# Performance work log

Measured on AMD Instinct MI355X. Metric: run time of the kernel, lower is better.

Reference implementation:

```python
import jax, jax.numpy as jnp
import numpy as np

G, N_PER_G, V, H, DIN, DOUT, E = 1024, 64, 32, 128, 128, 10, 1048576
N = G * N_PER_G


def _lin(key, fan_in, fan_out):
    k1, k2 = jax.random.split(key)
    s = 1.0 / np.sqrt(fan_in)
    return (jax.random.uniform(k1, (fan_in, fan_out), jnp.float32, -s, s),
            jax.random.uniform(k2, (fan_out,), jnp.float32, -s, s))


def setup_inputs() -> dict:
    key = jax.random.key(0)
    ks = jax.random.split(key, 16)
    x = jax.random.normal(ks[0], (N, DIN), jnp.float32)
    # random edges constrained within each graph's contiguous node block
    gid = jax.random.randint(ks[1], (E,), 0, G)
    src = gid * N_PER_G + jax.random.randint(ks[2], (E,), 0, N_PER_G)
    dst = gid * N_PER_G + jax.random.randint(ks[3], (E,), 0, N_PER_G)
    edge_index = jnp.stack([src, dst]).astype(jnp.int64)
    batch = jnp.repeat(jnp.arange(G, dtype=jnp.int64), N_PER_G)
    edge_weights = jnp.ones((G, N_PER_G, V), jnp.float32) / V  # uniform init
    vemb = jax.random.normal(ks[4], (G, V, H), jnp.float32)
    vemb = vemb / jnp.linalg.norm(vemb, axis=-1, keepdims=True)
    W_emb, b_emb = _lin(ks[5], DIN, H)
    W_gcn, b_gcn = _lin(ks[6], H, H)
    aff_W1, aff_b1 = _lin(ks[7], H, H)
    aff_W2, aff_b2 = _lin(ks[8], H, H)
    vn_W1, vn_b1 = _lin(ks[9], H, H)
    vn_W2, vn_b2 = _lin(ks[10], H, H)
    mlp_W1, mlp_b1 = _lin(ks[11], H, H)
    mlp_W2, mlp_b2 = _lin(ks[12], H, DOUT)
    return dict(x=x, edge_index=edge_index, batch=batch, edge_weights=edge_weights,
                vemb=vemb, W_emb=W_emb, b_emb=b_emb, W_gcn=W_gcn, b_gcn=b_gcn,
                aff_W1=aff_W1, aff_b1=aff_b1, aff_W2=aff_W2, aff_b2=aff_b2,
                vn_W1=vn_W1, vn_b1=vn_b1, vn_W2=vn_W2, vn_b2=vn_b2,
                mlp_W1=mlp_W1, mlp_b1=mlp_b1, mlp_W2=mlp_W2, mlp_b2=mlp_b2)


def reference(x, edge_index, batch, edge_weights, vemb, W_emb, b_emb, W_gcn, b_gcn,
              aff_W1, aff_b1, aff_W2, aff_b2, vn_W1, vn_b1, vn_W2, vn_b2,
              mlp_W1, mlp_b1, mlp_W2, mlp_b2):
    n_nodes = x.shape[0]
    g, n, v = edge_weights.shape
    h = x @ W_emb + b_emb                                   # node embedding
    # GCNConv with self-loops and symmetric normalization
    hw = h @ W_gcn
    sl = jnp.arange(n_nodes)
    s = jnp.concatenate([edge_index[0], sl])
    d = jnp.concatenate([edge_index[1], sl])
    deg = jax.ops.segment_sum(jnp.ones_like(d, dtype=h.dtype), d, num_segments=n_nodes)
    inv = jax.lax.rsqrt(jnp.maximum(deg, 1.0))
    msg = hw[s] * (inv[s] * inv[d])[:, None]                # [E+N, H]
    h = jax.nn.relu(jax.ops.segment_sum(msg, d, num_segments=n_nodes) + b_gcn)
    # affinity MLP
    aff = jax.nn.relu(h @ aff_W1 + aff_b1) @ aff_W2 + aff_b2
    hg = h.reshape(g, n, -1)
    affg = aff.reshape(g, n, -1)
    # attention vs fixed normalized virtual-node embeddings
    att = jnp.einsum('gnh,gvh->gnv', affg, vemb) / jnp.sqrt(jnp.asarray(hg.shape[-1], h.dtype))
    ew = edge_weights * (1.0 + jax.nn.sigmoid(att))
    rs = ew.sum(axis=-1, keepdims=True)
    ew = ew / jnp.where(rs == 0, 1.0, rs)                   # row-normalize
    vn = jnp.einsum('gnv,gnh->gvh', ew, hg)                 # weighted scatter-pool
    vn = jax.nn.relu(vn @ vn_W1 + vn_b1) @ vn_W2 + vn_b2
    gf = vn.mean(axis=1)                                    # [G, H]
    return jax.nn.relu(gf @ mlp_W1 + mlp_b1) @ mlp_W2 + mlp_b2
```

## Files before the change

### kernel.cpp

```cpp
#include <hip/hip_runtime.h>
#include <hip/hip_bf16.h>
#include <cstddef>


#define EDGES 1048576
#define TS 72
#define AS 64
#define VS 136
#define BS 40

typedef __attribute__((ext_vector_type(8))) short short8;
typedef __attribute__((ext_vector_type(4))) float f32x4;
typedef __hip_bfloat16 bf;
struct __align__(8) bf4 { bf v[4]; };

__device__ __forceinline__ int foff(int nt, int ks, int l15, int kofs) {
    return (nt * 4 + ks) * 512 + l15 * 32 + kofs;
}

__global__ __launch_bounds__(256) void conv(
    const float* __restrict__ W_emb, const float* __restrict__ W_gcn,
    const float* __restrict__ b_emb, const float* __restrict__ aff_W1,
    const float* __restrict__ vn_W1, const float* __restrict__ vn_W2,
    const float* __restrict__ aff_W2,
    bf* __restrict__ gWb, bf* __restrict__ gW2f, float* __restrict__ bfold,
    unsigned* __restrict__ Cnt)
{
    int b = blockIdx.x, t = threadIdx.x;
    if (b < 4) {
        __shared__ float we[32 * 128];
        int k0 = b * 32;
        for (int i = t; i < 4096; i += 256) we[i] = W_emb[k0 * 128 + i];
        __syncthreads();
        int kk = t >> 3, jg = t & 7;
        float acc[16] = {};
        for (int m = 0; m < 128; ++m) {
            float a = we[kk * 128 + m];
            const float4* wr = (const float4*)(W_gcn + m * 128 + jg * 16);
            float4 w0 = wr[0], w1 = wr[1], w2 = wr[2], w3 = wr[3];
            acc[0]  += a * w0.x; acc[1]  += a * w0.y; acc[2]  += a * w0.z; acc[3]  += a * w0.w;
            acc[4]  += a * w1.x; acc[5]  += a * w1.y; acc[6]  += a * w1.z; acc[7]  += a * w1.w;
            acc[8]  += a * w2.x; acc[9]  += a * w2.y; acc[10] += a * w2.z; acc[11] += a * w2.w;
            acc[12] += a * w3.x; acc[13] += a * w3.y; acc[14] += a * w3.z; acc[15] += a * w3.w;
        }
        int k = k0 + kk;
        for (int jj = 0; jj < 16; ++jj) {
            int j = jg * 16 + jj;
            int off = ((j >> 4) * 4 + (k >> 5)) * 512 + (j & 15) * 32 + (k & 31);
            gWb[off] = __float2bfloat16(acc[jj]);
        }
    } else if (b == 4) {
        if (t < 128) {
            float acc = 0.f;
            for (int m = 0; m < 128; ++m) acc += b_emb[m] * W_gcn[m * 128 + t];
            bfold[t] = acc;
        }
        for (int i = t; i < 1024; i += 256) Cnt[i] = 0u;
    } else if (b < 8) {
        const float* src = (b == 5) ? aff_W1 : (b == 6) ? vn_W1 : vn_W2;
        bf* dst = gWb + (size_t)(b - 4) * 16384;
        for (int i = t; i < 16384; i += 256) {
            int n = i >> 7, k = i & 127;
            int off = ((n >> 4) * 4 + (k >> 5)) * 512 + (n & 15) * 32 + (k & 31);
            dst[off] = __float2bfloat16(src[k * 128 + n]);
        }
    } else {
        for (int i = t; i < 16384; i += 256) {
            int n = i >> 7, k = i & 127;
            int off = ((n >> 4) * 4 + (k >> 5)) * 512 + (n & 15) * 32 + (k & 31);
            gW2f[off] = __float2bfloat16(aff_W2[n * 128 + k]);
        }
    }
}

__global__ __launch_bounds__(256) void scat(const int* __restrict__ ei,
                                            unsigned* __restrict__ Cnt,
                                            unsigned short* __restrict__ sorted)
{
    __shared__ unsigned lh[1024];
    __shared__ unsigned sBase[1024];
    int t = threadIdx.x, b = blockIdx.x;
    for (int i = t; i < 1024; i += 256) lh[i] = 0;
    __syncthreads();
    unsigned er[16];
    int base = b * 4096;
#pragma unroll
    for (int i = 0; i < 16; ++i) {
        int e = base + i * 256 + t;
        int s = ei[e], d = ei[EDGES + e];
        unsigned g = (unsigned)s >> 6;
        er[i] = (g << 12) | (unsigned)((d & 63) << 6) | (unsigned)(s & 63);
        atomicAdd(&lh[g], 1u);
    }
    __syncthreads();
    for (int i = t; i < 1024; i += 256) {
        unsigned c = lh[i];
        if (c) sBase[i] = atomicAdd(&Cnt[i], c);
    }
    __syncthreads();
    for (int i = t; i < 1024; i += 256) lh[i] = 0;
    __syncthreads();
#pragma unroll
    for (int i = 0; i < 16; ++i) {
        unsigned g = er[i] >> 12;
        unsigned r = atomicAdd(&lh[g], 1u);
        unsigned p = sBase[g] + r;
        if (p < 2048) sorted[(size_t)g * 2048 + p] = (unsigned short)(er[i] & 0xFFFu);
    }
}

__global__ __launch_bounds__(256) void prepS(
    const float* __restrict__ vemb, const float* __restrict__ aff_b2,
    const bf* __restrict__ gW2f, bf* __restrict__ gS, float* __restrict__ gbatt)
{
    __shared__ __align__(16) bf sV[32 * VS];
    const int t = threadIdx.x, g = blockIdx.x;
    const int wv = t >> 6, lane = t & 63, l15 = lane & 15, q = lane >> 4;
    const int kofs = q * 8;
    const float4* gv = (const float4*)(vemb + (size_t)g * 4096);
#pragma unroll
    for (int tt = 0; tt < 4; ++tt) {
        int i = t + tt * 256;
        int v = i >> 5, o4 = i & 31;
        float4 w = gv[i];
        bf4 tv;
        tv.v[0] = __float2bfloat16(w.x); tv.v[1] = __float2bfloat16(w.y);
        tv.v[2] = __float2bfloat16(w.z); tv.v[3] = __float2bfloat16(w.w);
        *(bf4*)(sV + v * VS + o4 * 4) = tv;
    }
    __syncthreads();
    {
        int v = t >> 3, sg = t & 7;
        float s = 0.f;
        const bf* pv = sV + v * VS + sg * 16;
        const float* pb = aff_b2 + sg * 16;
#pragma unroll
        for (int o = 0; o < 16; ++o) s += pb[o] * __bfloat162float(pv[o]);
        s += __shfl_xor(s, 1); s += __shfl_xor(s, 2); s += __shfl_xor(s, 4);
        if (sg == 0) gbatt[g * 32 + v] = s;
    }
    {
        const int mt = wv & 1, nb = (wv >> 1) * 4;
        f32x4 acc[4] = {};
#pragma unroll
        for (int ks = 0; ks < 4; ++ks) {
            short8 a = *(const short8*)(sV + (mt * 16 + l15) * VS + ks * 32 + kofs);
#pragma unroll
            for (int nt = 0; nt < 4; ++nt) {
                short8 bb = *(const short8*)(gW2f + foff(nb + nt, ks, l15, kofs));
                acc[nt] = __builtin_amdgcn_mfma_f32_16x16x32_bf16(a, bb, acc[nt], 0, 0, 0);
            }
        }
#pragma unroll
        for (int nt = 0; nt < 4; ++nt)
#pragma unroll
            for (int r = 0; r < 4; ++r) {
                int v = mt * 16 + q * 4 + r;
                int k = (nb + nt) * 16 + l15;
                int off = ((v >> 4) * 4 + (k >> 5)) * 512 + (v & 15) * 32 + (k & 31);
                gS[(size_t)g * 4096 + off] = __float2bfloat16(acc[nt][r]);
            }
    }
}

__device__ __forceinline__ void gemmA8(const short8 A[4], const bf* __restrict__ gW,
                                       int l15, int kofs, f32x4 acc[8])
{
#pragma unroll
    for (int hf = 0; hf < 2; ++hf) {
        short8 b[4], bn[4];
#pragma unroll
        for (int nt = 0; nt < 4; ++nt)
            b[nt] = *(const short8*)(gW + foff(hf * 4 + nt, 0, l15, kofs));
#pragma unroll
        for (int ks = 0; ks < 4; ++ks) {
            if (ks < 3)
#pragma unroll
                for (int nt = 0; nt < 4; ++nt)
                    bn[nt] = *(const short8*)(gW + foff(hf * 4 + nt, ks + 1, l15, kofs));
#pragma unroll
            for (int nt = 0; nt < 4; ++nt)
                acc[hf * 4 + nt] = __builtin_amdgcn_mfma_f32_16x16x32_bf16(
                    A[ks], b[nt], acc[hf * 4 + nt], 0, 0, 0);
#pragma unroll
            for (int nt = 0; nt < 4; ++nt) b[nt] = bn[nt];
        }
    }
}

__device__ __forceinline__ void gemmA4(const short8 A[4], const bf* __restrict__ gW,
                                       int ntb, int l15, int kofs, f32x4 acc[4])
{
    short8 b[4], bn[4];
#pragma unroll
    for (int nt = 0; nt < 4; ++nt)
        b[nt] = *(const short8*)(gW + foff(ntb + nt, 0, l15, kofs));
#pragma unroll
    for (int ks = 0; ks < 4; ++ks) {
        if (ks < 3)
#pragma unroll
            for (int nt = 0; nt < 4; ++nt)
                bn[nt] = *(const short8*)(gW + foff(ntb + nt, ks + 1, l15, kofs));
#pragma unroll
        for (int nt = 0; nt < 4; ++nt)
            acc[nt] = __builtin_amdgcn_mfma_f32_16x16x32_bf16(A[ks], b[nt], acc[nt], 0, 0, 0);
#pragma unroll
        for (int nt = 0; nt < 4; ++nt) b[nt] = bn[nt];
    }
}

__device__ __forceinline__ void bounceA(const float vals[8][4], bf* slab,
                                        int q, int l15, short8 A[4])
{
#pragma unroll
    for (int ks = 0; ks < 4; ++ks) {
#pragma unroll
        for (int h = 0; h < 2; ++h)
#pragma unroll
            for (int r = 0; r < 4; ++r)
                slab[(q * 4 + r) * BS + h * 16 + l15] = __float2bfloat16(vals[ks * 2 + h][r]);
        A[ks] = *(const short8*)(slab + l15 * BS + q * 8);
    }
}

__global__ __launch_bounds__(256, 4) void fused_graph(
    const float* __restrict__ x, const float* __restrict__ edge_w,
    const bf* __restrict__ gWb, const float* __restrict__ bfold,
    const float* __restrict__ b_gcn, const float* __restrict__ aff_b1,
    const float* __restrict__ vn_b1, const float* __restrict__ vn_b2,
    const bf* __restrict__ gS, const float* __restrict__ gbatt,
    const unsigned short* __restrict__ sorted, const unsigned* __restrict__ Cnt,
    float* __restrict__ gfout)
{
    __shared__ __align__(16) bf sT [128 * TS];
    __shared__ __align__(16) bf sAdj[64 * AS];
    __shared__ __align__(16) bf sBounce[4 * 16 * BS];
    __shared__ __align__(16) bf sVn[32 * VS];
    __shared__ float sInv[64];

    const int tid = threadIdx.x;
    const int g = blockIdx.x;
    const int wv = tid >> 6;
    const int lane = tid & 63;
    const int l15 = lane & 15;
    const int q = lane >> 4;
    const int kofs = q * 8;
    bf* slab = sBounce + wv * (16 * BS);
    float* sGfp = (float*)sBounce;
    unsigned* cnt = (unsigned*)sVn;

    {
        uint4* c4 = (uint4*)cnt;
        c4[tid] = make_uint4(0, 0, 0, 0);
    }
    __syncthreads();
    {
        unsigned ecnt = Cnt[g]; if (ecnt > 2048) ecnt = 2048;
        const unsigned short* seg = sorted + (size_t)g * 2048;
        for (unsigned i = tid; i < ecnt; i += 256) {
            unsigned w = seg[i];
            atomicAdd(&cnt[(w >> 6) * 16 + ((w & 63u) >> 2)], 1u << ((w & 3u) * 8));
        }
    }
    __syncthreads();
    {
        int row = tid >> 2, q4 = tid & 3;
        float rs = 0.f;
#pragma unroll
        for (int w4 = 0; w4 < 4; ++w4) {
            unsigned wd = cnt[row * 16 + q4 * 4 + w4];
            bf4 tv;
#pragma unroll
            for (int j = 0; j < 4; ++j) {
                int c = (q4 * 4 + w4) * 4 + j;
                float v = (float)((wd >> (j * 8)) & 255u) + (c == row ? 1.f : 0.f);
                rs += v;
                tv.v[j] = __float2bfloat16(v);
            }
            *(bf4*)(sAdj + row * AS + (q4 * 4 + w4) * 4) = tv;
        }
        rs += __shfl_xor(rs, 1);
        rs += __shfl_xor(rs, 2);
        if (q4 == 0) sInv[row] = rsqrtf(rs);
    }
    __syncthreads();

    {
        const float4* xrow = (const float4*)(x + ((size_t)g * 64 + 16 * wv + l15) * 128);
        short8 A[4];
#pragma unroll
        for (int ks = 0; ks < 4; ++ks) {
            float4 a0 = xrow[ks * 8 + q * 2];
            float4 a1 = xrow[ks * 8 + q * 2 + 1];
            union { short8 v; bf e[8]; } u;
            u.e[0] = __float2bfloat16(a0.x); u.e[1] = __float2bfloat16(a0.y);
            u.e[2] = __float2bfloat16(a0.z); u.e[3] = __float2bfloat16(a0.w);
            u.e[4] = __float2bfloat16(a1.x); u.e[5] = __float2bfloat16(a1.y);
            u.e[6] = __float2bfloat16(a1.z); u.e[7] = __float2bfloat16(a1.w);
            A[ks] = u.v;
        }
        f32x4 acc[8] = {};
        gemmA8(A, gWb, l15, kofs, acc);
        float bf_[8];
#pragma unroll
        for (int nt = 0; nt < 8; ++nt) bf_[nt] = bfold[nt * 16 + l15];
        float iv[4];
#pragma unroll
        for (int r = 0; r < 4; ++r) iv[r] = sInv[16 * wv + q * 4 + r];
#pragma unroll
        for (int nt = 0; nt < 8; ++nt) {
            bf4 tv;
#pragma unroll
            for (int r = 0; r < 4; ++r)
                tv.v[r] = __float2bfloat16((acc[nt][r] + bf_[nt]) * iv[r]);
            *(bf4*)(sT + (nt * 16 + l15) * TS + 16 * wv + q * 4) = tv;
        }
    }
    __syncthreads();

    float hvals[8][4];
    {
        f32x4 acc[8] = {};
#pragma unroll
        for (int ks = 0; ks < 2; ++ks) {
            short8 a = *(const short8*)(sAdj + (16 * wv + l15) * AS + ks * 32 + kofs);
#pragma unroll
            for (int nt = 0; nt < 8; ++nt) {
                short8 bb = *(const short8*)(sT + (nt * 16 + l15) * TS + ks * 32 + kofs);
                acc[nt] = __builtin_amdgcn_mfma_f32_16x16x32_bf16(a, bb, acc[nt], 0, 0, 0);
            }
        }
        float iv[4];
#pragma unroll
        for (int r = 0; r < 4; ++r) iv[r] = sInv[16 * wv + q * 4 + r];
#pragma unroll
        for (int nt = 0; nt < 8; ++nt) {
            float bg = b_gcn[nt * 16 + l15];
#pragma unroll
            for (int r = 0; r < 4; ++r)
                hvals[nt][r] = fmaxf(acc[nt][r] * iv[r] + bg, 0.f);
        }
    }
    __syncthreads();

    short8 Ah[4];
    {
#pragma unroll
        for (int nt = 0; nt < 8; ++nt) {
            bf4 tv;
#pragma unroll
            for (int r = 0; r < 4; ++r) tv.v[r] = __float2bfloat16(hvals[nt][r]);
            *(bf4*)(sT + (nt * 16 + l15) * TS + 16 * wv + q * 4) = tv;
        }
        bounceA(hvals, slab, q, l15, Ah);
    }

    short8 Aa[4];
    {
        f32x4 acc[8] = {};
        gemmA8(Ah, gWb + 16384, l15, kofs, acc);
        float av[8][4];
#pragma unroll
        for (int nt = 0; nt < 8; ++nt) {
            float ba = aff_b1[nt * 16 + l15];
#pragma unroll
            for (int r = 0; r < 4; ++r) av[nt][r] = fmaxf(acc[nt][r] + ba, 0.f);
        }
        bounceA(av, slab, q, l15, Aa);
    }

    {
        short8 Sf[8];
#pragma unroll
        for (int nt = 0; nt < 2; ++nt)
#pragma unroll
            for (int ks = 0; ks < 4; ++ks)
                Sf[nt * 4 + ks] = *(const short8*)(gS + (size_t)g * 4096 + foff(nt, ks, l15, kofs));
        float ewv[2][4];
#pragma unroll
        for (int nt = 0; nt < 2; ++nt)
#pragma unroll
            for (int r = 0; r < 4; ++r)
                ewv[nt][r] = edge_w[(size_t)g * 2048 + (16 * wv + q * 4 + r) * 32 + nt * 16 + l15];
        float bt[2] = { gbatt[g * 32 + l15], gbatt[g * 32 + 16 + l15] };
        f32x4 acc[2] = {};
#pragma unroll
        for (int ks = 0; ks < 4; ++ks) {
            acc[0] = __builtin_amdgcn_mfma_f32_16x16x32_bf16(Aa[ks], Sf[ks],     acc[0], 0, 0, 0);
            acc[1] = __builtin_amdgcn_mfma_f32_16x16x32_bf16(Aa[ks], Sf[4 + ks], acc[1], 0, 0, 0);
        }
        const float sc = 0.08838834764831845f;
        float e[2][4];
#pragma unroll
        for (int r = 0; r < 4; ++r) {
#pragma unroll
            for (int nt = 0; nt < 2; ++nt) {
                float att = (acc[nt][r] + bt[nt]) * sc;
                e[nt][r] = ewv[nt][r] * (1.f + 1.f / (1.f + __expf(-att)));
            }
            float rs = e[0][r] + e[1][r];
            rs += __shfl_xor(rs, 1); rs += __shfl_xor(rs, 2);
            rs += __shfl_xor(rs, 4); rs += __shfl_xor(rs, 8);
            float ri = (rs == 0.f) ? 1.f : 1.f / rs;
            e[0][r] *= ri; e[1][r] *= ri;
        }
#pragma unroll
        for (int nt = 0; nt < 2; ++nt) {
            bf4 tv;
#pragma unroll
            for (int r = 0; r < 4; ++r) tv.v[r] = __float2bfloat16(e[nt][r]);
            *(bf4*)(sAdj + (nt * 16 + l15) * AS + 16 * wv + q * 4) = tv;
        }
    }
    __syncthreads();

    const int mb = wv & 1, hf = wv >> 1;
    {
        f32x4 acc[4] = {};
#pragma unroll
        for (int ks = 0; ks < 2; ++ks) {
            short8 a = *(const short8*)(sAdj + (mb * 16 + l15) * AS + ks * 32 + kofs);
#pragma unroll
            for (int nt = 0; nt < 4; ++nt) {
                short8 bb = *(const short8*)(sT + (hf * 64 + nt * 16 + l15) * TS + ks * 32 + kofs);
                acc[nt] = __builtin_amdgcn_mfma_f32_16x16x32_bf16(a, bb, acc[nt], 0, 0, 0);
            }
        }
#pragma unroll
        for (int nt = 0; nt < 4; ++nt)
#pragma unroll
            for (int r = 0; r < 4; ++r)
                sVn[(mb * 16 + q * 4 + r) * VS + hf * 64 + nt * 16 + l15] =
                    __float2bfloat16(acc[nt][r]);
    }
    __syncthreads();

    bf* vn1 = sT;
    {
        short8 A[4];
#pragma unroll
        for (int ks = 0; ks < 4; ++ks)
            A[ks] = *(const short8*)(sVn + (mb * 16 + l15) * VS + ks * 32 + kofs);
        f32x4 acc[4] = {};
        gemmA4(A, gWb + 2 * 16384, hf * 4, l15, kofs, acc);
#pragma unroll
        for (int nt = 0; nt < 4; ++nt) {
            float b1 = vn_b1[hf * 64 + nt * 16 + l15];
#pragma unroll
            for (int r = 0; r < 4; ++r)
                vn1[(mb * 16 + q * 4 + r) * VS + hf * 64 + nt * 16 + l15] =
                    __float2bfloat16(fmaxf(acc[nt][r] + b1, 0.f));
        }
    }
    __syncthreads();

    {
        short8 A[4];
#pragma unroll
        for (int ks = 0; ks < 4; ++ks)
            A[ks] = *(const short8*)(vn1 + (mb * 16 + l15) * VS + ks * 32 + kofs);
        f32x4 acc[4] = {};
        gemmA4(A, gWb + 3 * 16384, hf * 4, l15, kofs, acc);
#pragma unroll
        for (int nt = 0; nt < 4; ++nt) {
            float b2 = vn_b2[hf * 64 + nt * 16 + l15];
            float p = (acc[nt][0] + b2) + (acc[nt][1] + b2) + (acc[nt][2] + b2) + (acc[nt][3] + b2);
            p += __shfl_xor(p, 16);
            p += __shfl_xor(p, 32);
            if (q == 0) sGfp[mb * 128 + hf * 64 + nt * 16 + l15] = p;
        }
    }
    __syncthreads();
    if (tid < 128)
        gfout[(size_t)g * 128 + tid] = (sGfp[tid] + sGfp[128 + tid]) * 0.03125f;
}

__global__ __launch_bounds__(256) void tail_mlp(const float* __restrict__ gf,
                                                const float* __restrict__ W1,
                                                const float* __restrict__ b1,
                                                const float* __restrict__ W2,
                                                const float* __restrict__ b2,
                                                float* __restrict__ out)
{
    __shared__ float z[2][128];
    int tid = threadIdx.x;
    int half = tid >> 7, o = tid & 127;
    const float* gr = gf + (blockIdx.x * 2 + half) * 128;
    float a = b1[o];
#pragma unroll 4
    for (int k = 0; k < 128; ++k) a = fmaf(gr[k], W1[k * 128 + o], a);
    z[half][o] = fmaxf(a, 0.f);
    __syncthreads();
    if (tid < 160) {
        int grp = tid >> 3, jg = tid & 7;
        int r2 = grp / 10, oo = grp % 10;
        float p = 0.f;
#pragma unroll
        for (int t = 0; t < 16; ++t) {
            int j = jg * 16 + t;
            p = fmaf(z[r2][j], W2[j * 10 + oo], p);
        }
        p += __shfl_xor(p, 1); p += __shfl_xor(p, 2); p += __shfl_xor(p, 4);
        if (jg == 0) out[(blockIdx.x * 2 + r2) * 10 + oo] = p + b2[oo];
    }
}

extern "C" void kernel_launch(void* const* d_in, const int* in_sizes, int n_in,
                              void* d_out, int out_size, void* d_ws, size_t ws_size,
                              hipStream_t stream)
{
    const float* x       = (const float*)d_in[0];
    const int*   ei      = (const int*)  d_in[1];
    const float* edge_w  = (const float*)d_in[3];
    const float* vemb    = (const float*)d_in[4];
    const float* W_emb   = (const float*)d_in[5];
    const float* b_emb   = (const float*)d_in[6];
    const float* W_gcn   = (const float*)d_in[7];
    const float* b_gcn   = (const float*)d_in[8];
    const float* aff_W1  = (const float*)d_in[9];
    const float* aff_b1  = (const float*)d_in[10];
    const float* aff_W2  = (const float*)d_in[11];
    const float* aff_b2  = (const float*)d_in[12];
    const float* vn_W1   = (const float*)d_in[13];
    const float* vn_b1   = (const float*)d_in[14];
    const float* vn_W2   = (const float*)d_in[15];
    const float* vn_b2   = (const float*)d_in[16];
    const float* mlp_W1  = (const float*)d_in[17];
    const float* mlp_b1  = (const float*)d_in[18];
    const float* mlp_W2  = (const float*)d_in[19];
    const float* mlp_b2  = (const float*)d_in[20];

    char* ws = (char*)d_ws;
    unsigned short* sorted = (unsigned short*)ws;
    unsigned* Cnt   = (unsigned*)(ws + (4u << 20));
    bf*       gWb   = (bf*)     (ws + (4u << 20) + 65536);
    float*    bfold = (float*)  (ws + (4u << 20) + 65536 + 131072);
    bf*       gW2f  = (bf*)     (ws + (4u << 20) + 262144);
    bf*       gS    = (bf*)     (ws + (5u << 20));
    float*    gbatt = (float*)  (ws + (13u << 20));
    float*    gfbuf = (float*)  (ws + (14u << 20));

    conv <<<dim3(9),    dim3(256), 0, stream>>>(W_emb, W_gcn, b_emb, aff_W1,
                                                vn_W1, vn_W2, aff_W2,
                                                gWb, gW2f, bfold, Cnt);
    scat <<<dim3(256),  dim3(256), 0, stream>>>(ei, Cnt, sorted);
    prepS<<<dim3(1024), dim3(256), 0, stream>>>(vemb, aff_b2, gW2f, gS, gbatt);
    fused_graph<<<dim3(1024), dim3(256), 0, stream>>>(
        x, edge_w, gWb, bfold, b_gcn, aff_b1, vn_b1, vn_b2,
        gS, gbatt, sorted, Cnt, gfbuf);
    tail_mlp<<<dim3(512), dim3(256), 0, stream>>>(
        gfbuf, mlp_W1, mlp_b1, mlp_W2, mlp_b2, (float*)d_out);
}
```

Before: 223.1 us.

## Merge weight prep into one launch and fuse tail MLP into graph kernel

Combines the conv and prepS kernels into a single prep launch: the vemb@aff_W2^T product now converts aff_W2 to bf16 on the fly instead of reading a pre-transposed buffer, and W_emb@W_gcn is computed with MFMA. The tail MLP is folded into the end of fused_graph, so each graph block writes its final 10 outputs directly. This removes two kernel launches and the gf round trip through global memory. In exchange each prep block redundantly converts aff_W2 from fp32, and the per-graph MLP adds serial work at the end of fused_graph.

```diff
diff --git a/kernel.cpp b/kernel.cpp
--- a/kernel.cpp
+++ b/kernel.cpp
@@ -18,58 +18,118 @@
     return (nt * 4 + ks) * 512 + l15 * 32 + kofs;
 }
 
-__global__ __launch_bounds__(256) void conv(
-    const float* __restrict__ W_emb, const float* __restrict__ W_gcn,
-    const float* __restrict__ b_emb, const float* __restrict__ aff_W1,
-    const float* __restrict__ vn_W1, const float* __restrict__ vn_W2,
-    const float* __restrict__ aff_W2,
-    bf* __restrict__ gWb, bf* __restrict__ gW2f, float* __restrict__ bfold,
-    unsigned* __restrict__ Cnt)
-{
-    int b = blockIdx.x, t = threadIdx.x;
-    if (b < 4) {
-        __shared__ float we[32 * 128];
-        int k0 = b * 32;
-        for (int i = t; i < 4096; i += 256) we[i] = W_emb[k0 * 128 + i];
+__device__ __forceinline__ short8 cvt8(const float* p) {
+    float4 v0 = *(const float4*)p, v1 = *(const float4*)(p + 4);
+    union { short8 v; bf e[8]; } u;
+    u.e[0] = __float2bfloat16(v0.x); u.e[1] = __float2bfloat16(v0.y);
+    u.e[2] = __float2bfloat16(v0.z); u.e[3] = __float2bfloat16(v0.w);
+    u.e[4] = __float2bfloat16(v1.x); u.e[5] = __float2bfloat16(v1.y);
+    u.e[6] = __float2bfloat16(v1.z); u.e[7] = __float2bfloat16(v1.w);
+    return u.v;
+}
+
+__global__ __launch_bounds__(256) void prep(
+    const float* __restrict__ vemb, const float* __restrict__ aff_b2,
+    const float* __restrict__ aff_W2, const float* __restrict__ W_emb,
+    const float* __restrict__ W_gcn, const float* __restrict__ b_emb,
+    const float* __restrict__ aff_W1, const float* __restrict__ vn_W1,
+    const float* __restrict__ vn_W2,
+    bf* __restrict__ gWb, float* __restrict__ bfold,
+    bf* __restrict__ gS, float* __restrict__ gbatt, unsigned* __restrict__ Cnt)
+{
+    const int b = blockIdx.x, t = threadIdx.x;
+    const int wv = t >> 6, lane = t & 63, l15 = lane & 15, q = lane >> 4;
+    const int kofs = q * 8;
+    if (b < 1024) {
+        __shared__ __align__(16) bf sV[32 * VS];
+        const float4* gv = (const float4*)(vemb + (size_t)b * 4096);
+#pragma unroll
+        for (int tt = 0; tt < 4; ++tt) {
+            int i = t + tt * 256;
+            int v = i >> 5, o4 = i & 31;
+            float4 w = gv[i];
+            bf4 tv;
+            tv.v[0] = __float2bfloat16(w.x); tv.v[1] = __float2bfloat16(w.y);
+            tv.v[2] = __float2bfloat16(w.z); tv.v[3] = __float2bfloat16(w.w);
+            *(bf4*)(sV + v * VS + o4 * 4) = tv;
+        }
         __syncthreads();
-        int kk = t >> 3, jg = t & 7;
-        float acc[16] = {};
-        for (int m = 0; m < 128; ++m) {
-            float a = we[kk * 128 + m];
-            const float4* wr = (const float4*)(W_gcn + m * 128 + jg * 16);
-            float4 w0 = wr[0], w1 = wr[1], w2 = wr[2], w3 = wr[3];
-            acc[0]  += a * w0.x; acc[1]  += a * w0.y; acc[2]  += a * w0.z; acc[3]  += a * w0.w;
-            acc[4]  += a * w1.x; acc[5]  += a * w1.y; acc[6]  += a * w1.z; acc[7]  += a * w1.w;
-            acc[8]  += a * w2.x; acc[9]  += a * w2.y; acc[10] += a * w2.z; acc[11] += a * w2.w;
-            acc[12] += a * w3.x; acc[13] += a * w3.y; acc[14] += a * w3.z; acc[15] += a * w3.w;
-        }
-        int k = k0 + kk;
-        for (int jj = 0; jj < 16; ++jj) {
-            int j = jg * 16 + jj;
-            int off = ((j >> 4) * 4 + (k >> 5)) * 512 + (j & 15) * 32 + (k & 31);
-            gWb[off] = __float2bfloat16(acc[jj]);
-        }
-    } else if (b == 4) {
+        {
+            int v = t >> 3, sg = t & 7;
+            float s = 0.f;
+            const bf* pv = sV + v * VS + sg * 16;
+            const float* pb = aff_b2 + sg * 16;
+#pragma unroll
+            for (int o = 0; o < 16; ++o) s += pb[o] * __bfloat162float(pv[o]);
+            s += __shfl_xor(s, 1); s += __shfl_xor(s, 2); s += __shfl_xor(s, 4);
+            if (sg == 0) gbatt[b * 32 + v] = s;
+        }
+        {
+            const int mt = wv & 1, nb = (wv >> 1) * 4;
+            f32x4 acc[4] = {};
+#pragma unroll
+            for (int ks = 0; ks < 4; ++ks) {
+                short8 a = *(const short8*)(sV + (mt * 16 + l15) * VS + ks * 32 + kofs);
+#pragma unroll
+                for (int nt = 0; nt < 4; ++nt) {
+                    int n = (nb + nt) * 16 + l15;
+                    short8 bb = cvt8(aff_W2 + n * 128 + ks * 32 + kofs);
+                    acc[nt] = __builtin_amdgcn_mfma_f32_16x16x32_bf16(a, bb, acc[nt], 0, 0, 0);
+                }
+            }
+#pragma unroll
+            for (int nt = 0; nt < 4; ++nt)
+#pragma unroll
+                for (int r = 0; r < 4; ++r) {
+                    int v = mt * 16 + q * 4 + r;
+                    int k = (nb + nt) * 16 + l15;
+                    int off = ((v >> 4) * 4 + (k >> 5)) * 512 + (v & 15) * 32 + (k & 31);
+                    gS[(size_t)b * 4096 + off] = __float2bfloat16(acc[nt][r]);
+                }
+        }
+    } else if (b == 1024) {
         if (t < 128) {
             float acc = 0.f;
-            for (int m = 0; m < 128; ++m) acc += b_emb[m] * W_gcn[m * 128 + t];
+#pragma unroll 16
+            for (int m = 0; m < 128; ++m) acc = fmaf(b_emb[m], W_gcn[m * 128 + t], acc);
             bfold[t] = acc;
         }
-        for (int i = t; i < 1024; i += 256) Cnt[i] = 0u;
-    } else if (b < 8) {
-        const float* src = (b == 5) ? aff_W1 : (b == 6) ? vn_W1 : vn_W2;
-        bf* dst = gWb + (size_t)(b - 4) * 16384;
+#pragma unroll
+        for (int kt2 = 0; kt2 < 2; ++kt2) {
+            int kt = wv * 2 + kt2;
+            short8 Af[4];
+#pragma unroll
+            for (int ks = 0; ks < 4; ++ks)
+                Af[ks] = cvt8(W_emb + (kt * 16 + l15) * 128 + ks * 32 + kofs);
+#pragma unroll
+            for (int jt = 0; jt < 8; ++jt) {
+                f32x4 acc = {};
+#pragma unroll
+                for (int ks = 0; ks < 4; ++ks) {
+                    union { short8 v; bf e[8]; } u;
+#pragma unroll
+                    for (int i = 0; i < 8; ++i)
+                        u.e[i] = __float2bfloat16(W_gcn[(ks * 32 + kofs + i) * 128 + jt * 16 + l15]);
+                    acc = __builtin_amdgcn_mfma_f32_16x16x32_bf16(Af[ks], u.v, acc, 0, 0, 0);
+                }
+#pragma unroll
+                for (int r = 0; r < 4; ++r) {
+                    int k = kt * 16 + q * 4 + r;
+                    gWb[(jt * 4 + (k >> 5)) * 512 + l15 * 32 + (k & 31)] =
+                        __float2bfloat16(acc[r]);
+                }
+            }
+        }
+    } else if (b < 1028) {
+        const float* src = (b == 1025) ? aff_W1 : (b == 1026) ? vn_W1 : vn_W2;
+        bf* dst = gWb + (size_t)(b - 1024) * 16384;
         for (int i = t; i < 16384; i += 256) {
             int n = i >> 7, k = i & 127;
             int off = ((n >> 4) * 4 + (k >> 5)) * 512 + (n & 15) * 32 + (k & 31);
             dst[off] = __float2bfloat16(src[k * 128 + n]);
         }
     } else {
-        for (int i = t; i < 16384; i += 256) {
-            int n = i >> 7, k = i & 127;
-            int off = ((n >> 4) * 4 + (k >> 5)) * 512 + (n & 15) * 32 + (k & 31);
-            gW2f[off] = __float2bfloat16(aff_W2[n * 128 + k]);
-        }
+        for (int i = t; i < 1024; i += 256) Cnt[i] = 0u;
     }
 }
 
@@ -109,60 +169,6 @@
     }
 }
 
-__global__ __launch_bounds__(256) void prepS(
-    const float* __restrict__ vemb, const float* __restrict__ aff_b2,
-    const bf* __restrict__ gW2f, bf* __restrict__ gS, float* __restrict__ gbatt)
-{
-    __shared__ __align__(16) bf sV[32 * VS];
-    const int t = threadIdx.x, g = blockIdx.x;
-    const int wv = t >> 6, lane = t & 63, l15 = lane & 15, q = lane >> 4;
-    const int kofs = q * 8;
-    const float4* gv = (const float4*)(vemb + (size_t)g * 4096);
-#pragma unroll
-    for (int tt = 0; tt < 4; ++tt) {
-        int i = t + tt * 256;
-        int v = i >> 5, o4 = i & 31;
-        float4 w = gv[i];
-        bf4 tv;
-        tv.v[0] = __float2bfloat16(w.x); tv.v[1] = __float2bfloat16(w.y);
-        tv.v[2] = __float2bfloat16(w.z); tv.v[3] = __float2bfloat16(w.w);
-        *(bf4*)(sV + v * VS + o4 * 4) = tv;
-    }
-    __syncthreads();
-    {
-        int v = t >> 3, sg = t & 7;
-        float s = 0.f;
-        const bf* pv = sV + v * VS + sg * 16;
-        const float* pb = aff_b2 + sg * 16;
-#pragma unroll
-        for (int o = 0; o < 16; ++o) s += pb[o] * __bfloat162float(pv[o]);
-        s += __shfl_xor(s, 1); s += __shfl_xor(s, 2); s += __shfl_xor(s, 4);
-        if (sg == 0) gbatt[g * 32 + v] = s;
-    }
-    {
-        const int mt = wv & 1, nb = (wv >> 1) * 4;
-        f32x4 acc[4] = {};
-#pragma unroll
-        for (int ks = 0; ks < 4; ++ks) {
-            short8 a = *(const short8*)(sV + (mt * 16 + l15) * VS + ks * 32 + kofs);
-#pragma unroll
-            for (int nt = 0; nt < 4; ++nt) {
-                short8 bb = *(const short8*)(gW2f + foff(nb + nt, ks, l15, kofs));
-                acc[nt] = __builtin_amdgcn_mfma_f32_16x16x32_bf16(a, bb, acc[nt], 0, 0, 0);
-            }
-        }
-#pragma unroll
-        for (int nt = 0; nt < 4; ++nt)
-#pragma unroll
-            for (int r = 0; r < 4; ++r) {
-                int v = mt * 16 + q * 4 + r;
-                int k = (nb + nt) * 16 + l15;
-                int off = ((v >> 4) * 4 + (k >> 5)) * 512 + (v & 15) * 32 + (k & 31);
-                gS[(size_t)g * 4096 + off] = __float2bfloat16(acc[nt][r]);
-            }
-    }
-}
-
 __device__ __forceinline__ void gemmA8(const short8 A[4], const bf* __restrict__ gW,
                                        int l15, int kofs, f32x4 acc[8])
 {
@@ -229,8 +235,10 @@
     const float* __restrict__ b_gcn, const float* __restrict__ aff_b1,
     const float* __restrict__ vn_b1, const float* __restrict__ vn_b2,
     const bf* __restrict__ gS, const float* __restrict__ gbatt,
+    const float* __restrict__ mlp_W1, const float* __restrict__ mlp_b1,
+    const float* __restrict__ mlp_W2, const float* __restrict__ mlp_b2,
     const unsigned short* __restrict__ sorted, const unsigned* __restrict__ Cnt,
-    float* __restrict__ gfout)
+    float* __restrict__ out)
 {
     __shared__ __align__(16) bf sT [128 * TS];
     __shared__ __align__(16) bf sAdj[64 * AS];
@@ -471,37 +479,26 @@
         }
     }
     __syncthreads();
-    if (tid < 128)
-        gfout[(size_t)g * 128 + tid] = (sGfp[tid] + sGfp[128 + tid]) * 0.03125f;
-}
-
-__global__ __launch_bounds__(256) void tail_mlp(const float* __restrict__ gf,
-                                                const float* __restrict__ W1,
-                                                const float* __restrict__ b1,
-                                                const float* __restrict__ W2,
-                                                const float* __restrict__ b2,
-                                                float* __restrict__ out)
-{
-    __shared__ float z[2][128];
-    int tid = threadIdx.x;
-    int half = tid >> 7, o = tid & 127;
-    const float* gr = gf + (blockIdx.x * 2 + half) * 128;
-    float a = b1[o];
-#pragma unroll 4
-    for (int k = 0; k < 128; ++k) a = fmaf(gr[k], W1[k * 128 + o], a);
-    z[half][o] = fmaxf(a, 0.f);
+    if (tid < 128) sGfp[tid] = (sGfp[tid] + sGfp[128 + tid]) * 0.03125f;
+    __syncthreads();
+    if (tid < 128) {
+        float a = mlp_b1[tid];
+#pragma unroll 16
+        for (int k = 0; k < 128; ++k) a = fmaf(sGfp[k], mlp_W1[k * 128 + tid], a);
+        sGfp[128 + tid] = fmaxf(a, 0.f);
+    }
     __syncthreads();
     if (tid < 160) {
-        int grp = tid >> 3, jg = tid & 7;
-        int r2 = grp / 10, oo = grp % 10;
+        int o = tid >> 4, jg = tid & 15;
         float p = 0.f;
 #pragma unroll
-        for (int t = 0; t < 16; ++t) {
-            int j = jg * 16 + t;
-            p = fmaf(z[r2][j], W2[j * 10 + oo], p);
-        }
-        p += __shfl_xor(p, 1); p += __shfl_xor(p, 2); p += __shfl_xor(p, 4);
-        if (jg == 0) out[(blockIdx.x * 2 + r2) * 10 + oo] = p + b2[oo];
+        for (int t2 = 0; t2 < 8; ++t2) {
+            int j = jg * 8 + t2;
+            p = fmaf(sGfp[128 + j], mlp_W2[j * 10 + o], p);
+        }
+        p += __shfl_xor(p, 1); p += __shfl_xor(p, 2);
+        p += __shfl_xor(p, 4); p += __shfl_xor(p, 8);
+        if (jg == 0) out[g * 10 + o] = p + mlp_b2[o];
     }
 }
 
@@ -535,19 +532,14 @@
     unsigned* Cnt   = (unsigned*)(ws + (4u << 20));
     bf*       gWb   = (bf*)     (ws + (4u << 20) + 65536);
     float*    bfold = (float*)  (ws + (4u << 20) + 65536 + 131072);
-    bf*       gW2f  = (bf*)     (ws + (4u << 20) + 262144);
     bf*       gS    = (bf*)     (ws + (5u << 20));
     float*    gbatt = (float*)  (ws + (13u << 20));
-    float*    gfbuf = (float*)  (ws + (14u << 20));
-
-    conv <<<dim3(9),    dim3(256), 0, stream>>>(W_emb, W_gcn, b_emb, aff_W1,
-                                                vn_W1, vn_W2, aff_W2,
-                                                gWb, gW2f, bfold, Cnt);
-    scat <<<dim3(256),  dim3(256), 0, stream>>>(ei, Cnt, sorted);
-    prepS<<<dim3(1024), dim3(256), 0, stream>>>(vemb, aff_b2, gW2f, gS, gbatt);
+
+    prep<<<dim3(1029), dim3(256), 0, stream>>>(
+        vemb, aff_b2, aff_W2, W_emb, W_gcn, b_emb, aff_W1, vn_W1, vn_W2,
+        gWb, bfold, gS, gbatt, Cnt);
+    scat<<<dim3(256), dim3(256), 0, stream>>>(ei, Cnt, sorted);
     fused_graph<<<dim3(1024), dim3(256), 0, stream>>>(
         x, edge_w, gWb, bfold, b_gcn, aff_b1, vn_b1, vn_b2,
-        gS, gbatt, sorted, Cnt, gfbuf);
-    tail_mlp<<<dim3(512), dim3(256), 0, stream>>>(
-        gfbuf, mlp_W1, mlp_b1, mlp_W2, mlp_b2, (float*)d_out);
-}
+        gS, gbatt, mlp_W1, mlp_b1, mlp_W2, mlp_b2, sorted, Cnt, (float*)d_out);
+}
```

New measurement: 213.5 us. 1.05x faster.
